# Optimization experiments

Hardware: AMD Instinct MI355X
Metric: run time of the kernel (lower is better)

## Reference

```python
import jax, jax.numpy as jnp
import numpy as np

B, Q, K, A, H, C, O = 32, 512, 512, 256, 8, 32, 256  # batch, queries, keys, channels, heads, head_dim, out_dim


def setup_inputs() -> dict:
    key = jax.random.key(0)
    ks = jax.random.split(key, 12)
    s = 0.02
    return {
        "q_data": jax.random.normal(ks[0], (B, Q, A), jnp.float32),
        "m_data": jax.random.normal(ks[1], (B, K, A), jnp.float32),
        "bias": jax.random.normal(ks[2], (B, 1, 1, K), jnp.float32),
        "nonbatched_bias": jax.random.normal(ks[3], (H, Q, K), jnp.float32),
        "batched_bias": jax.random.normal(ks[4], (B, H, Q, K), jnp.float32),
        "query_w": jax.random.normal(ks[5], (A, H, C), jnp.float32) * s,
        "key_w": jax.random.normal(ks[6], (A, H, C), jnp.float32) * s,
        "value_w": jax.random.normal(ks[7], (A, H, C), jnp.float32) * s,
        "gating_w": jax.random.normal(ks[8], (A, H, C), jnp.float32) * s,
        "gating_b": jnp.ones((H, C), jnp.float32),
        "output_w": jax.random.normal(ks[9], (H, C, O), jnp.float32) * s,
        "output_b": jnp.zeros((O,), jnp.float32),
    }


def reference(q_data, m_data, bias, nonbatched_bias, batched_bias,
              query_w, key_w, value_w, gating_w, gating_b, output_w, output_b):
    key_scale = query_w.shape[-1] ** -0.5
    q = jnp.einsum('bqa,ahc->bqhc', q_data, query_w) * key_scale
    k = jnp.einsum('bka,ahc->bkhc', m_data, key_w)
    v = jnp.einsum('bka,ahc->bkhc', m_data, value_w)
    logits = jnp.einsum('bqhc,bkhc->bhqk', q, k) + bias
    logits = logits + nonbatched_bias[None] + batched_bias
    weights = jax.nn.softmax(logits, axis=-1)
    weighted_avg = jnp.einsum('bhqk,bkhc->bqhc', weights, v)
    gate = jax.nn.sigmoid(jnp.einsum('bqc,chv->bqhv', q_data, gating_w) + gating_b)
    weighted_avg = weighted_avg * gate
    return jnp.einsum('bqhc,hco->bqo', weighted_avg, output_w) + output_b
```

## Files before the change

kernel.cpp:

```cpp
#include <hip/hip_runtime.h>
#include <cstdint>
#include <cstddef>


typedef __attribute__((ext_vector_type(8))) short short8;
typedef __attribute__((ext_vector_type(4))) float f32x4;
typedef __attribute__((ext_vector_type(4))) unsigned int u32x4;
typedef __attribute__((ext_vector_type(2))) unsigned int u32x2;

#define DEVFN static __device__ __forceinline__
#define L2E 1.4426950408889634f

DEVFN float b2f(unsigned int bits16) {
  return __builtin_bit_cast(float, bits16 << 16);
}
DEVFN unsigned int pack2(float a, float b) {
  unsigned int r;
  asm("v_cvt_pk_bf16_f32 %0, %1, %2" : "=v"(r) : "v"(a), "v"(b));
  return r;
}
DEVFN f32x4 mfma16(short8 a, short8 b, f32x4 c) {
  return __builtin_amdgcn_mfma_f32_16x16x32_bf16(a, b, c, 0, 0, 0);
}
#define GLOAD_LDS16_NT(gp, lp)                                     \
  __builtin_amdgcn_global_load_lds(                                \
      (const __attribute__((address_space(1))) void*)(gp),         \
      (__attribute__((address_space(3))) void*)(lp), 16, 0, 2)

__global__ __launch_bounds__(256) void wtrans_kernel(
    const float* __restrict__ qw, const float* __restrict__ kw,
    const float* __restrict__ vw, const float* __restrict__ gw,
    const float* __restrict__ ow,
    unsigned short* __restrict__ wtq, unsigned short* __restrict__ wtk,
    unsigned short* __restrict__ wtv, unsigned short* __restrict__ wtg,
    unsigned short* __restrict__ wt3)
{
  const int matid = blockIdx.x >> 4;
  const int tile  = blockIdx.x & 15;
  const float* src = (matid == 0) ? qw : (matid == 1) ? kw : (matid == 2) ? vw
                   : (matid == 3) ? gw : ow;
  unsigned short* dst = (matid == 0) ? wtq : (matid == 1) ? wtk : (matid == 2) ? wtv
                      : (matid == 3) ? wtg : wt3;
  const int tr = (tile >> 2) * 64, tc = (tile & 3) * 64;
  __shared__ unsigned short T[64 * 72];
  const int t = threadIdx.x;
  {
    const int row = t >> 2, cb = (t & 3) * 16;
#pragma unroll
    for (int ii = 0; ii < 4; ++ii) {
      f32x4 v = *(const f32x4*)&src[(size_t)(tr + row) * 256 + tc + cb + ii * 4];
      u32x2 p; p.x = pack2(v.x, v.y); p.y = pack2(v.z, v.w);
      *(u32x2*)&T[row * 72 + cb + ii * 4] = p;
    }
  }
  __syncthreads();
  {
    const int c0 = t >> 2, rb = (t & 3) * 16;
    unsigned short vals[16];
#pragma unroll
    for (int m = 0; m < 16; ++m) vals[m] = T[(rb + m) * 72 + c0];
    u32x4 s0, s1;
    s0.x = (unsigned)vals[0]  | ((unsigned)vals[1]  << 16);
    s0.y = (unsigned)vals[2]  | ((unsigned)vals[3]  << 16);
    s0.z = (unsigned)vals[4]  | ((unsigned)vals[5]  << 16);
    s0.w = (unsigned)vals[6]  | ((unsigned)vals[7]  << 16);
    s1.x = (unsigned)vals[8]  | ((unsigned)vals[9]  << 16);
    s1.y = (unsigned)vals[10] | ((unsigned)vals[11] << 16);
    s1.z = (unsigned)vals[12] | ((unsigned)vals[13] << 16);
    s1.w = (unsigned)vals[14] | ((unsigned)vals[15] << 16);
    unsigned short* dp = &dst[(size_t)(tc + c0) * 256 + tr + rb];
    *(u32x4*)dp = s0;
    *(u32x4*)(dp + 8) = s1;
  }
}

__global__ __launch_bounds__(512, 4) void proj_kernel(
    const float* __restrict__ q_data, const float* __restrict__ m_data,
    const unsigned short* __restrict__ wtq, const unsigned short* __restrict__ wtk,
    const unsigned short* __restrict__ wtv, const unsigned short* __restrict__ wtg,
    const float* __restrict__ gating_b,
    unsigned short* __restrict__ qp, unsigned short* __restrict__ kp,
    unsigned short* __restrict__ vp, unsigned short* __restrict__ gate)
{
  const int bid = blockIdx.x;
  const bool mside = bid >= 256;
  const int r0 = (mside ? bid - 256 : bid) * 64;
  const float* inp = mside ? m_data : q_data;
  __shared__ unsigned short Alds[64 * 264];
  __shared__ unsigned short Wlds[2][256 * 40];
  const int t = threadIdx.x;
  const int lane = t & 63, wave = t >> 6;
  const int l15 = lane & 15, g = lane >> 4;
  const int stripe = wave & 3, nhalf = wave >> 2;

  {
    const int row = t >> 3, cb = (t & 7) * 32;
    const float* ip = &inp[(size_t)(r0 + row) * 256 + cb];
#pragma unroll
    for (int i = 0; i < 4; ++i) {
      f32x4 a0 = *(const f32x4*)&ip[i * 8];
      f32x4 a1 = *(const f32x4*)&ip[i * 8 + 4];
      u32x4 pk;
      pk.x = pack2(a0.x, a0.y); pk.y = pack2(a0.z, a0.w);
      pk.z = pack2(a1.x, a1.y); pk.w = pack2(a1.z, a1.w);
      *(u32x4*)&Alds[row * 264 + cb + i * 8] = pk;
    }
  }

  const unsigned short* wt0 = mside ? wtk : wtq;
  const unsigned short* wt1 = mside ? wtv : wtg;
  const int wrow = t & 255, whalf = t >> 8;

  {
    const u32x4* wsrc = (const u32x4*)&wt0[(size_t)wrow * 256 + whalf * 16];
    u32x4 a = wsrc[0], b = wsrc[1];
    *(u32x4*)&Wlds[0][wrow * 40 + whalf * 16 + 0] = a;
    *(u32x4*)&Wlds[0][wrow * 40 + whalf * 16 + 8] = b;
  }

  f32x4 acc[8];
#pragma unroll
  for (int j = 0; j < 8; ++j) acc[j] = f32x4{0.f, 0.f, 0.f, 0.f};

  const int arow = (stripe * 16 + l15) * 264 + 8 * g;
  const int grow = r0 + stripe * 16 + l15;
  const int ob = grow >> 9, oq = grow & 511;

#pragma unroll
  for (int s = 0; s < 16; ++s) {
    const int p = s & 1;
    __syncthreads();
    u32x4 nw0, nw1;
    if (s < 15) {
      const unsigned short* wt = (s + 1 < 8) ? wt0 : wt1;
      const u32x4* wsrc =
          (const u32x4*)&wt[(size_t)wrow * 256 + ((s + 1) & 7) * 32 + whalf * 16];
      nw0 = wsrc[0]; nw1 = wsrc[1];
    }
    const int ks = s & 7;
    short8 bf = __builtin_bit_cast(short8, *(const u32x4*)&Alds[arow + ks * 32]);
#pragma unroll
    for (int j = 0; j < 8; ++j) {
      short8 wf = __builtin_bit_cast(short8,
          *(const u32x4*)&Wlds[p][((nhalf * 8 + j) * 16 + l15) * 40 + 8 * g]);
      acc[j] = mfma16(wf, bf, acc[j]);
    }
    if (s < 15) {
      *(u32x4*)&Wlds[p ^ 1][wrow * 40 + whalf * 16 + 0] = nw0;
      *(u32x4*)&Wlds[p ^ 1][wrow * 40 + whalf * 16 + 8] = nw1;
    }
    if (s == 7 || s == 15) {
      const int oi = s >> 3;
      const float QS = 0.17677669529663687f * 1.4426950408889634f;
#pragma unroll
      for (int j = 0; j < 8; ++j) {
        const int n0 = (nhalf * 8 + j) * 16 + 4 * g;
        const int h = n0 >> 5, c0 = n0 & 31;
        const size_t idx = ((size_t)(ob * 8 + h) * 512 + oq) * 32 + c0;
        f32x4 v = acc[j];
        if (!mside) {
          if (oi == 0) {
            u32x2 st;
            st.x = pack2(v.x * QS, v.y * QS);
            st.y = pack2(v.z * QS, v.w * QS);
            *(u32x2*)&qp[idx] = st;
          } else {
            f32x4 gb = *(const f32x4*)&gating_b[n0];
            f32x4 gv;
            gv.x = 1.0f / (1.0f + exp2f(-(v.x + gb.x) * L2E));
            gv.y = 1.0f / (1.0f + exp2f(-(v.y + gb.y) * L2E));
            gv.z = 1.0f / (1.0f + exp2f(-(v.z + gb.z) * L2E));
            gv.w = 1.0f / (1.0f + exp2f(-(v.w + gb.w) * L2E));
            u32x2 st;
            st.x = pack2(gv.x, gv.y); st.y = pack2(gv.z, gv.w);
            *(u32x2*)&gate[idx] = st;
          }
        } else {
          u32x2 st;
          st.x = pack2(v.x, v.y); st.y = pack2(v.z, v.w);
          if (oi == 0) *(u32x2*)&kp[idx] = st;
          else         *(u32x2*)&vp[idx] = st;
        }
        acc[j] = f32x4{0.f, 0.f, 0.f, 0.f};
      }
    }
  }
}

__global__ __launch_bounds__(512, 2) void attn_kernel(
    const unsigned short* __restrict__ qp, const unsigned short* __restrict__ kp,
    const unsigned short* __restrict__ vp,
    const float* __restrict__ bias, const float* __restrict__ nbias,
    const float* __restrict__ bbias,
    unsigned short* __restrict__ wa)
{
  const int bid = blockIdx.x;
  const int h = bid & 7;
  const int b = bid >> 3;
  const int bh = bid;
  const int t = threadIdx.x;
  const int lane = t & 63, wave = t >> 6;
  const int l15 = lane & 15, g = lane >> 4;

  __shared__ unsigned short Klds[512 * 32];
  __shared__ unsigned short Vt[32 * 520];
  __shared__ float Bb[2][8192];
  __shared__ float Bk[512];

  const float* bbb_bh = bbias + (size_t)bh * 262144;
  const int qc = lane >> 3, sl = lane & 7;
  const float* wsrc0 = bbb_bh + (size_t)(wave * 32 + qc) * 512 + ((sl ^ qc) << 2);

#pragma unroll
  for (int i = 0; i < 4; ++i)
    GLOAD_LDS16_NT(wsrc0 + i * 4096,      &Bb[0][(wave * 4 + i) * 256]);
#pragma unroll
  for (int i = 0; i < 4; ++i)
    GLOAD_LDS16_NT(wsrc0 + i * 4096 + 32, &Bb[1][(wave * 4 + i) * 256]);

  {
    const int row = t;
    const u32x4* ks = (const u32x4*)&kp[((size_t)bh * 512 + row) * 32];
    u32x4 k0 = ks[0], k1 = ks[1], k2 = ks[2], k3 = ks[3];
    *(u32x4*)&Klds[row * 32 + 0]  = k0;
    *(u32x4*)&Klds[row * 32 + 8]  = k1;
    *(u32x4*)&Klds[row * 32 + 16] = k2;
    *(u32x4*)&Klds[row * 32 + 24] = k3;
    const u32x4* vs = (const u32x4*)&vp[((size_t)bh * 512 + row) * 32];
#pragma unroll
    for (int cc = 0; cc < 4; ++cc) {
      u32x4 vv = vs[cc];
      unsigned int dw0 = vv.x, dw1 = vv.y, dw2 = vv.z, dw3 = vv.w;
      const int c = cc * 8;
      Vt[(c + 0) * 520 + row] = (unsigned short)(dw0 & 0xffff);
      Vt[(c + 1) * 520 + row] = (unsigned short)(dw0 >> 16);
      Vt[(c + 2) * 520 + row] = (unsigned short)(dw1 & 0xffff);
      Vt[(c + 3) * 520 + row] = (unsigned short)(dw1 >> 16);
      Vt[(c + 4) * 520 + row] = (unsigned short)(dw2 & 0xffff);
      Vt[(c + 5) * 520 + row] = (unsigned short)(dw2 >> 16);
      Vt[(c + 6) * 520 + row] = (unsigned short)(dw3 & 0xffff);
      Vt[(c + 7) * 520 + row] = (unsigned short)(dw3 >> 16);
    }
    if (t < 128) {
      f32x4 bv = *(const f32x4*)&bias[(size_t)b * 512 + t * 4];
      bv.x *= L2E; bv.y *= L2E; bv.z *= L2E; bv.w *= L2E;
      *(f32x4*)&Bk[t * 4] = bv;
    }
  }

  const int pib = ((g & 1) << 4) | ((g >> 1) << 3);
  const bool godd = (g & 1) != 0;
  const int sw0 = (g ^ (l15 & 7)) << 2;
  const int sw1 = ((g + 4) ^ (l15 & 7)) << 2;
  const int bq0 = (wave * 32 + l15) * 32;
  const int bq1 = bq0 + 16 * 32;

  f32x4 Cn00, Cn01, Cn10, Cn11;
  {
    const float* nn = nbias + (size_t)h * 262144
                    + (size_t)(wave * 32 + l15) * 512 + 4 * g;
    Cn00 = *(const f32x4*)nn;
    Cn01 = *(const f32x4*)(nn + 16);
    Cn10 = *(const f32x4*)(nn + 16 * 512);
    Cn11 = *(const f32x4*)(nn + 16 * 512 + 16);
  }

  short8 qf0, qf1;
  f32x4 acc[2][2];
  float l_part[2] = {0.f, 0.f};

  __syncthreads();

  for (int tok = 0; tok < 32; ++tok) {
    const int pass = tok >> 4, kt = tok & 15, p = tok & 1;
    const int k0 = kt * 32;

    if (kt == 0) {
      const int qbase = pass * 256 + wave * 32;
      qf0 = __builtin_bit_cast(short8,
          *(const u32x4*)&qp[((size_t)bh * 512 + qbase + l15) * 32 + 8 * g]);
      qf1 = __builtin_bit_cast(short8,
          *(const u32x4*)&qp[((size_t)bh * 512 + qbase + 16 + l15) * 32 + 8 * g]);
#pragma unroll
      for (int ct = 0; ct < 2; ++ct)
#pragma unroll
        for (int qt = 0; qt < 2; ++qt) acc[ct][qt] = f32x4{0.f, 0.f, 0.f, 0.f};
      l_part[0] = 0.f; l_part[1] = 0.f;
    }

    short8 kf0 = __builtin_bit_cast(short8, *(const u32x4*)&Klds[(k0 + l15) * 32 + 8 * g]);
    short8 kf1 = __builtin_bit_cast(short8, *(const u32x4*)&Klds[(k0 + 16 + l15) * 32 + 8 * g]);
    short8 vf0 = __builtin_bit_cast(short8, *(const u32x4*)&Vt[l15 * 520 + k0 + pib]);
    short8 vf1 = __builtin_bit_cast(short8, *(const u32x4*)&Vt[(16 + l15) * 520 + k0 + pib]);
    f32x4 bks0 = *(const f32x4*)&Bk[k0 + 4 * g];
    f32x4 bks1 = *(const f32x4*)&Bk[k0 + 16 + 4 * g];
    const float* bp = Bb[p];
    f32x4 bb00 = *(const f32x4*)&bp[bq0 + sw0];
    f32x4 bb01 = *(const f32x4*)&bp[bq0 + sw1];
    f32x4 bb10 = *(const f32x4*)&bp[bq1 + sw0];
    f32x4 bb11 = *(const f32x4*)&bp[bq1 + sw1];
    asm volatile("s_waitcnt lgkmcnt(0)" ::: "memory");
    __builtin_amdgcn_sched_barrier(0);

    f32x4 Nn00, Nn01, Nn10, Nn11;
    if (tok < 31) {
      const int nt = tok + 1;
      const float* nn = nbias + (size_t)h * 262144
          + (size_t)((nt >> 4) * 256 + wave * 32 + l15) * 512 + (nt & 15) * 32 + 4 * g;
      Nn00 = *(const f32x4*)nn;
      Nn01 = *(const f32x4*)(nn + 16);
      Nn10 = *(const f32x4*)(nn + 16 * 512);
      Nn11 = *(const f32x4*)(nn + 16 * 512 + 16);
    }

    if (tok < 30) {
      const int ft = tok + 2;
      const float* ws = wsrc0 + (size_t)(ft >> 4) * 131072 + (ft & 15) * 32;
#pragma unroll
      for (int i = 0; i < 4; ++i)
        GLOAD_LDS16_NT(ws + (size_t)i * 4096, &Bb[p][(wave * 4 + i) * 256]);
    }

    __builtin_amdgcn_s_setprio(1);
#pragma unroll
    for (int qt = 0; qt < 2; ++qt) {
      f32x4 bb0 = qt ? bb10 : bb00;
      f32x4 bb1 = qt ? bb11 : bb01;
      f32x4 nb0 = qt ? Cn10 : Cn00;
      f32x4 nb1 = qt ? Cn11 : Cn01;
      f32x4 c0 = bb0 * L2E + (nb0 * L2E + bks0);
      f32x4 c1 = bb1 * L2E + (nb1 * L2E + bks1);
      short8 qf = qt ? qf1 : qf0;
      f32x4 s0 = mfma16(kf0, qf, c0);
      f32x4 s1 = mfma16(kf1, qf, c1);
      f32x4 p0, p1;
      p0.x = exp2f(s0.x); p0.y = exp2f(s0.y);
      p0.z = exp2f(s0.z); p0.w = exp2f(s0.w);
      p1.x = exp2f(s1.x); p1.y = exp2f(s1.y);
      p1.z = exp2f(s1.z); p1.w = exp2f(s1.w);
      l_part[qt] += ((p0.x + p0.y) + (p0.z + p0.w)) +
                    ((p1.x + p1.y) + (p1.z + p1.w));
      unsigned int d0 = pack2(p0.x, p0.y), d1 = pack2(p0.z, p0.w);
      unsigned int e0 = pack2(p1.x, p1.y), e1 = pack2(p1.z, p1.w);
      unsigned int pd0 = __shfl_xor(d0, 16, 64), pd1 = __shfl_xor(d1, 16, 64);
      unsigned int pe0 = __shfl_xor(e0, 16, 64), pe1 = __shfl_xor(e1, 16, 64);
      u32x4 pfu;
      pfu.x = godd ? pe0 : d0;
      pfu.y = godd ? pe1 : d1;
      pfu.z = godd ? e0 : pd0;
      pfu.w = godd ? e1 : pd1;
      short8 pf = __builtin_bit_cast(short8, pfu);
      acc[0][qt] = mfma16(vf0, pf, acc[0][qt]);
      acc[1][qt] = mfma16(vf1, pf, acc[1][qt]);
    }
    __builtin_amdgcn_s_setprio(0);

    if (tok < 31) { Cn00 = Nn00; Cn01 = Nn01; Cn10 = Nn10; Cn11 = Nn11; }

    if (tok < 30)       asm volatile("s_waitcnt vmcnt(8)" ::: "memory");
    else if (tok == 30) asm volatile("s_waitcnt vmcnt(4)" ::: "memory");

    if (kt == 15) {
      const int qbase = pass * 256 + wave * 32;
      unsigned short* wab = wa + (size_t)bh * 512 * 32;
#pragma unroll
      for (int qt = 0; qt < 2; ++qt) {
        float l = l_part[qt];
        l += __shfl_xor(l, 16, 64);
        l += __shfl_xor(l, 32, 64);
        const float rl = 1.0f / l;
        const int q = qbase + qt * 16 + l15;
#pragma unroll
        for (int ct = 0; ct < 2; ++ct) {
          f32x4 v = acc[ct][qt];
          u32x2 st;
          st.x = pack2(v.x * rl, v.y * rl);
          st.y = pack2(v.z * rl, v.w * rl);
          *(u32x2*)&wab[q * 32 + ct * 16 + 4 * g] = st;
        }
      }
    }
  }
}

__global__ __launch_bounds__(256, 2) void outp_kernel(
    const unsigned short* __restrict__ wa, const unsigned short* __restrict__ gate,
    const unsigned short* __restrict__ wt3, const float* __restrict__ out_b,
    float* __restrict__ out)
{
  const int r0 = blockIdx.x * 32;
  const int t = threadIdx.x;
  const int lane = t & 63, wave = t >> 6;
  const int l15 = lane & 15, g = lane >> 4;
  const int stripe = wave & 1, half = wave >> 1;
  __shared__ unsigned short Wlds[2][256 * 40];

  const int grow = r0 + stripe * 16 + l15;
  const int b = grow >> 9, q = grow & 511;

  {
    const u32x4* wsrc = (const u32x4*)&wt3[(size_t)t * 256];
    u32x4 a = wsrc[0], bb = wsrc[1], c = wsrc[2], d = wsrc[3];
    *(u32x4*)&Wlds[0][t * 40 + 0]  = a;
    *(u32x4*)&Wlds[0][t * 40 + 8]  = bb;
    *(u32x4*)&Wlds[0][t * 40 + 16] = c;
    *(u32x4*)&Wlds[0][t * 40 + 24] = d;
  }
  size_t aidx = ((size_t)(b * 8 + 0) * 512 + q) * 32 + 8 * g;
  u32x4 cwv = *(const u32x4*)&wa[aidx];
  u32x4 cgv = *(const u32x4*)&gate[aidx];

  f32x4 acc[8];
#pragma unroll
  for (int j = 0; j < 8; ++j) acc[j] = f32x4{0.f, 0.f, 0.f, 0.f};

#pragma unroll
  for (int s = 0; s < 8; ++s) {
    const int p = s & 1;
    __syncthreads();
    u32x4 nw0, nw1, nw2, nw3, nwv, ngv;
    if (s < 7) {
      const u32x4* wsrc = (const u32x4*)&wt3[(size_t)t * 256 + (s + 1) * 32];
      nw0 = wsrc[0]; nw1 = wsrc[1]; nw2 = wsrc[2]; nw3 = wsrc[3];
      const size_t na = ((size_t)(b * 8 + s + 1) * 512 + q) * 32 + 8 * g;
      nwv = *(const u32x4*)&wa[na];
      ngv = *(const u32x4*)&gate[na];
    }
    float f0 = b2f(cwv.x & 0xffff) * b2f(cgv.x & 0xffff);
    float f1 = b2f(cwv.x >> 16)    * b2f(cgv.x >> 16);
    float f2 = b2f(cwv.y & 0xffff) * b2f(cgv.y & 0xffff);
    float f3 = b2f(cwv.y >> 16)    * b2f(cgv.y >> 16);
    float f4 = b2f(cwv.z & 0xffff) * b2f(cgv.z & 0xffff);
    float f5 = b2f(cwv.z >> 16)    * b2f(cgv.z >> 16);
    float f6 = b2f(cwv.w & 0xffff) * b2f(cgv.w & 0xffff);
    float f7 = b2f(cwv.w >> 16)    * b2f(cgv.w >> 16);
    u32x4 au;
    au.x = pack2(f0, f1); au.y = pack2(f2, f3);
    au.z = pack2(f4, f5); au.w = pack2(f6, f7);
    short8 af = __builtin_bit_cast(short8, au);
#pragma unroll
    for (int j = 0; j < 8; ++j) {
      short8 wf = __builtin_bit_cast(short8,
          *(const u32x4*)&Wlds[p][((half * 8 + j) * 16 + l15) * 40 + 8 * g]);
      acc[j] = mfma16(wf, af, acc[j]);
    }
    if (s < 7) {
      *(u32x4*)&Wlds[p ^ 1][t * 40 + 0]  = nw0;
      *(u32x4*)&Wlds[p ^ 1][t * 40 + 8]  = nw1;
      *(u32x4*)&Wlds[p ^ 1][t * 40 + 16] = nw2;
      *(u32x4*)&Wlds[p ^ 1][t * 40 + 24] = nw3;
      cwv = nwv; cgv = ngv;
    }
  }
#pragma unroll
  for (int j = 0; j < 8; ++j) {
    const int o0 = (half * 8 + j) * 16 + 4 * g;
    f32x4 ob4 = *(const f32x4*)&out_b[o0];
    f32x4 v = acc[j] + ob4;
    *(f32x4*)&out[(size_t)grow * 256 + o0] = v;
  }
}

extern "C" void kernel_launch(void* const* d_in, const int* in_sizes, int n_in,
                              void* d_out, int out_size, void* d_ws, size_t ws_size,
                              hipStream_t stream)
{
  const float* q_data   = (const float*)d_in[0];
  const float* m_data   = (const float*)d_in[1];
  const float* bias     = (const float*)d_in[2];
  const float* nbb      = (const float*)d_in[3];
  const float* bbb      = (const float*)d_in[4];
  const float* query_w  = (const float*)d_in[5];
  const float* key_w    = (const float*)d_in[6];
  const float* value_w  = (const float*)d_in[7];
  const float* gating_w = (const float*)d_in[8];
  const float* gating_b = (const float*)d_in[9];
  const float* output_w = (const float*)d_in[10];
  const float* output_b = (const float*)d_in[11];
  float* out = (float*)d_out;

  const size_t QP_B   = (size_t)32 * 8 * 512 * 32 * 2;
  const size_t GATE_B = (size_t)32 * 8 * 512 * 32 * 2;
  const size_t WT_B   = (size_t)256 * 256 * 2;

  char* ws = (char*)d_ws;
  unsigned short* qp  = (unsigned short*)(ws);
  unsigned short* kp  = (unsigned short*)(ws + QP_B);
  unsigned short* vp  = (unsigned short*)(ws + 2 * QP_B);
  unsigned short* wab = (unsigned short*)(ws + 3 * QP_B);
  unsigned short* gat = (unsigned short*)(ws + 4 * QP_B);
  unsigned short* wtq = (unsigned short*)(ws + 4 * QP_B + GATE_B);
  unsigned short* wtk = (unsigned short*)(ws + 4 * QP_B + GATE_B + WT_B);
  unsigned short* wtv = (unsigned short*)(ws + 4 * QP_B + GATE_B + 2 * WT_B);
  unsigned short* wtg = (unsigned short*)(ws + 4 * QP_B + GATE_B + 3 * WT_B);
  unsigned short* wt3 = (unsigned short*)(ws + 4 * QP_B + GATE_B + 4 * WT_B);
  const size_t need = 4 * QP_B + GATE_B + 5 * WT_B;
  if (ws_size < need) return;

  hipLaunchKernelGGL(wtrans_kernel, dim3(80), dim3(256), 0, stream,
                     query_w, key_w, value_w, gating_w, output_w,
                     wtq, wtk, wtv, wtg, wt3);
  hipLaunchKernelGGL(proj_kernel, dim3(512), dim3(512), 0, stream,
                     q_data, m_data, wtq, wtk, wtv, wtg, gating_b,
                     qp, kp, vp, gat);
  hipLaunchKernelGGL(attn_kernel, dim3(256), dim3(512), 0, stream,
                     qp, kp, vp, bias, nbb, bbb, wab);
  hipLaunchKernelGGL(outp_kernel, dim3(512), dim3(256), 0, stream,
                     wab, gat, wt3, output_b, out);
}
```

Baseline: 120.5 us.

## Widen key tile to 64 and single-buffer batched-bias staging in LDS

The attention main loop now handles 64 keys per iteration instead of 32, halving the trip count to 16. Each iteration issues four QK MFMAs and two PV MFMA pairs per query tile. The batched-bias staging changes from a double-buffered 32-column LDS layout to one 64-column per-wave buffer with a new XOR swizzle. The next tile is prefetched into that buffer after the current values are read into registers. The aim is to amortise per-iteration waits, loop overhead and load issue across more work. The cost is higher register use under 512-thread, 2-block launch bounds, a risk of spills, and a prefetch distance cut from two tiles to one.

New measurement: 121.1 us. About the same (+0.5%).

```diff
diff --git a/kernel.cpp b/kernel.cpp
--- a/kernel.cpp
+++ b/kernel.cpp
@@ -204,19 +204,17 @@
 
   __shared__ unsigned short Klds[512 * 32];
   __shared__ unsigned short Vt[32 * 520];
-  __shared__ float Bb[2][8192];
+  __shared__ float Bt[256 * 64];
   __shared__ float Bk[512];
 
   const float* bbb_bh = bbias + (size_t)bh * 262144;
-  const int qc = lane >> 3, sl = lane & 7;
-  const float* wsrc0 = bbb_bh + (size_t)(wave * 32 + qc) * 512 + ((sl ^ qc) << 2);
-
-#pragma unroll
-  for (int i = 0; i < 4; ++i)
-    GLOAD_LDS16_NT(wsrc0 + i * 4096,      &Bb[0][(wave * 4 + i) * 256]);
-#pragma unroll
-  for (int i = 0; i < 4; ++i)
-    GLOAD_LDS16_NT(wsrc0 + i * 4096 + 32, &Bb[1][(wave * 4 + i) * 256]);
+  const int qc4 = lane >> 4, sl16 = lane & 15;
+  const float* wbase = bbb_bh + (size_t)(wave * 32 + qc4) * 512;
+
+#pragma unroll
+  for (int c = 0; c < 8; ++c)
+    GLOAD_LDS16_NT(wbase + (size_t)(c * 4) * 512 + ((sl16 ^ ((c * 4 + qc4) & 15)) << 2),
+                   &Bt[(wave * 32 + c * 4) * 64]);
 
   {
     const int row = t;
@@ -250,32 +248,32 @@
 
   const int pib = ((g & 1) << 4) | ((g >> 1) << 3);
   const bool godd = (g & 1) != 0;
-  const int sw0 = (g ^ (l15 & 7)) << 2;
-  const int sw1 = ((g + 4) ^ (l15 & 7)) << 2;
-  const int bq0 = (wave * 32 + l15) * 32;
-  const int bq1 = bq0 + 16 * 32;
-
-  f32x4 Cn00, Cn01, Cn10, Cn11;
-  {
-    const float* nn = nbias + (size_t)h * 262144
-                    + (size_t)(wave * 32 + l15) * 512 + 4 * g;
-    Cn00 = *(const f32x4*)nn;
-    Cn01 = *(const f32x4*)(nn + 16);
-    Cn10 = *(const f32x4*)(nn + 16 * 512);
-    Cn11 = *(const f32x4*)(nn + 16 * 512 + 16);
+  const int tr0 = (wave * 32 + l15) * 64;
+  const int tr1 = tr0 + 16 * 64;
+
+  f32x4 Cn[2][4];
+  {
+    const float* nn0 = nbias + (size_t)h * 262144
+                     + (size_t)(wave * 32 + l15) * 512 + 4 * g;
+#pragma unroll
+    for (int qt = 0; qt < 2; ++qt)
+#pragma unroll
+      for (int kk = 0; kk < 4; ++kk)
+        Cn[qt][kk] = *(const f32x4*)(nn0 + (size_t)qt * 16 * 512 + kk * 16);
   }
 
   short8 qf0, qf1;
   f32x4 acc[2][2];
   float l_part[2] = {0.f, 0.f};
 
+  asm volatile("s_waitcnt vmcnt(0)" ::: "memory");
   __syncthreads();
 
-  for (int tok = 0; tok < 32; ++tok) {
-    const int pass = tok >> 4, kt = tok & 15, p = tok & 1;
-    const int k0 = kt * 32;
-
-    if (kt == 0) {
+  for (int tok = 0; tok < 16; ++tok) {
+    const int pass = tok >> 3, kt8 = tok & 7;
+    const int k0 = kt8 * 64;
+
+    if (kt8 == 0) {
       const int qbase = pass * 256 + wave * 32;
       qf0 = __builtin_bit_cast(short8,
           *(const u32x4*)&qp[((size_t)bh * 512 + qbase + l15) * 32 + 8 * g]);
@@ -288,79 +286,91 @@
       l_part[0] = 0.f; l_part[1] = 0.f;
     }
 
-    short8 kf0 = __builtin_bit_cast(short8, *(const u32x4*)&Klds[(k0 + l15) * 32 + 8 * g]);
-    short8 kf1 = __builtin_bit_cast(short8, *(const u32x4*)&Klds[(k0 + 16 + l15) * 32 + 8 * g]);
-    short8 vf0 = __builtin_bit_cast(short8, *(const u32x4*)&Vt[l15 * 520 + k0 + pib]);
-    short8 vf1 = __builtin_bit_cast(short8, *(const u32x4*)&Vt[(16 + l15) * 520 + k0 + pib]);
-    f32x4 bks0 = *(const f32x4*)&Bk[k0 + 4 * g];
-    f32x4 bks1 = *(const f32x4*)&Bk[k0 + 16 + 4 * g];
-    const float* bp = Bb[p];
-    f32x4 bb00 = *(const f32x4*)&bp[bq0 + sw0];
-    f32x4 bb01 = *(const f32x4*)&bp[bq0 + sw1];
-    f32x4 bb10 = *(const f32x4*)&bp[bq1 + sw0];
-    f32x4 bb11 = *(const f32x4*)&bp[bq1 + sw1];
+    short8 kf[4], vf[2][2];
+    f32x4 bks[4], bb0[4], bb1[4];
+#pragma unroll
+    for (int kk = 0; kk < 4; ++kk) {
+      kf[kk] = __builtin_bit_cast(short8,
+          *(const u32x4*)&Klds[(k0 + kk * 16 + l15) * 32 + 8 * g]);
+      bks[kk] = *(const f32x4*)&Bk[k0 + kk * 16 + 4 * g];
+      const int slot = ((kk * 4 + g) ^ l15) << 2;
+      bb0[kk] = *(const f32x4*)&Bt[tr0 + slot];
+      bb1[kk] = *(const f32x4*)&Bt[tr1 + slot];
+    }
+#pragma unroll
+    for (int ks = 0; ks < 2; ++ks) {
+      vf[0][ks] = __builtin_bit_cast(short8,
+          *(const u32x4*)&Vt[l15 * 520 + k0 + ks * 32 + pib]);
+      vf[1][ks] = __builtin_bit_cast(short8,
+          *(const u32x4*)&Vt[(16 + l15) * 520 + k0 + ks * 32 + pib]);
+    }
     asm volatile("s_waitcnt lgkmcnt(0)" ::: "memory");
     __builtin_amdgcn_sched_barrier(0);
 
-    f32x4 Nn00, Nn01, Nn10, Nn11;
-    if (tok < 31) {
+    if (tok < 15) {
+      const int ft = tok + 1;
+      const float* ws = wbase + (size_t)(ft >> 3) * 131072 + (ft & 7) * 64;
+#pragma unroll
+      for (int c = 0; c < 8; ++c)
+        GLOAD_LDS16_NT(ws + (size_t)(c * 4) * 512 + ((sl16 ^ ((c * 4 + qc4) & 15)) << 2),
+                       &Bt[(wave * 32 + c * 4) * 64]);
+    }
+    f32x4 Nn[2][4];
+    if (tok < 15) {
       const int nt = tok + 1;
-      const float* nn = nbias + (size_t)h * 262144
-          + (size_t)((nt >> 4) * 256 + wave * 32 + l15) * 512 + (nt & 15) * 32 + 4 * g;
-      Nn00 = *(const f32x4*)nn;
-      Nn01 = *(const f32x4*)(nn + 16);
-      Nn10 = *(const f32x4*)(nn + 16 * 512);
-      Nn11 = *(const f32x4*)(nn + 16 * 512 + 16);
-    }
-
-    if (tok < 30) {
-      const int ft = tok + 2;
-      const float* ws = wsrc0 + (size_t)(ft >> 4) * 131072 + (ft & 15) * 32;
-#pragma unroll
-      for (int i = 0; i < 4; ++i)
-        GLOAD_LDS16_NT(ws + (size_t)i * 4096, &Bb[p][(wave * 4 + i) * 256]);
+      const float* nn0 = nbias + (size_t)h * 262144
+          + (size_t)((nt >> 3) * 256 + wave * 32 + l15) * 512 + (nt & 7) * 64 + 4 * g;
+#pragma unroll
+      for (int qt = 0; qt < 2; ++qt)
+#pragma unroll
+        for (int kk = 0; kk < 4; ++kk)
+          Nn[qt][kk] = *(const f32x4*)(nn0 + (size_t)qt * 16 * 512 + kk * 16);
     }
 
     __builtin_amdgcn_s_setprio(1);
 #pragma unroll
     for (int qt = 0; qt < 2; ++qt) {
-      f32x4 bb0 = qt ? bb10 : bb00;
-      f32x4 bb1 = qt ? bb11 : bb01;
-      f32x4 nb0 = qt ? Cn10 : Cn00;
-      f32x4 nb1 = qt ? Cn11 : Cn01;
-      f32x4 c0 = bb0 * L2E + (nb0 * L2E + bks0);
-      f32x4 c1 = bb1 * L2E + (nb1 * L2E + bks1);
       short8 qf = qt ? qf1 : qf0;
-      f32x4 s0 = mfma16(kf0, qf, c0);
-      f32x4 s1 = mfma16(kf1, qf, c1);
-      f32x4 p0, p1;
-      p0.x = exp2f(s0.x); p0.y = exp2f(s0.y);
-      p0.z = exp2f(s0.z); p0.w = exp2f(s0.w);
-      p1.x = exp2f(s1.x); p1.y = exp2f(s1.y);
-      p1.z = exp2f(s1.z); p1.w = exp2f(s1.w);
-      l_part[qt] += ((p0.x + p0.y) + (p0.z + p0.w)) +
-                    ((p1.x + p1.y) + (p1.z + p1.w));
-      unsigned int d0 = pack2(p0.x, p0.y), d1 = pack2(p0.z, p0.w);
-      unsigned int e0 = pack2(p1.x, p1.y), e1 = pack2(p1.z, p1.w);
-      unsigned int pd0 = __shfl_xor(d0, 16, 64), pd1 = __shfl_xor(d1, 16, 64);
-      unsigned int pe0 = __shfl_xor(e0, 16, 64), pe1 = __shfl_xor(e1, 16, 64);
-      u32x4 pfu;
-      pfu.x = godd ? pe0 : d0;
-      pfu.y = godd ? pe1 : d1;
-      pfu.z = godd ? e0 : pd0;
-      pfu.w = godd ? e1 : pd1;
-      short8 pf = __builtin_bit_cast(short8, pfu);
-      acc[0][qt] = mfma16(vf0, pf, acc[0][qt]);
-      acc[1][qt] = mfma16(vf1, pf, acc[1][qt]);
+      f32x4 pr[4];
+#pragma unroll
+      for (int kk = 0; kk < 4; ++kk) {
+        f32x4 bb = qt ? bb1[kk] : bb0[kk];
+        f32x4 c = bb * L2E + (Cn[qt][kk] * L2E + bks[kk]);
+        f32x4 s = mfma16(kf[kk], qf, c);
+        f32x4 pe;
+        pe.x = exp2f(s.x); pe.y = exp2f(s.y);
+        pe.z = exp2f(s.z); pe.w = exp2f(s.w);
+        l_part[qt] += (pe.x + pe.y) + (pe.z + pe.w);
+        pr[kk] = pe;
+      }
+#pragma unroll
+      for (int ks = 0; ks < 2; ++ks) {
+        f32x4 p0 = pr[2 * ks], p1 = pr[2 * ks + 1];
+        unsigned int d0 = pack2(p0.x, p0.y), d1 = pack2(p0.z, p0.w);
+        unsigned int e0 = pack2(p1.x, p1.y), e1 = pack2(p1.z, p1.w);
+        unsigned int pd0 = __shfl_xor(d0, 16, 64), pd1 = __shfl_xor(d1, 16, 64);
+        unsigned int pe0 = __shfl_xor(e0, 16, 64), pe1 = __shfl_xor(e1, 16, 64);
+        u32x4 pfu;
+        pfu.x = godd ? pe0 : d0;
+        pfu.y = godd ? pe1 : d1;
+        pfu.z = godd ? e0 : pd0;
+        pfu.w = godd ? e1 : pd1;
+        short8 pf = __builtin_bit_cast(short8, pfu);
+        acc[0][qt] = mfma16(vf[0][ks], pf, acc[0][qt]);
+        acc[1][qt] = mfma16(vf[1][ks], pf, acc[1][qt]);
+      }
     }
     __builtin_amdgcn_s_setprio(0);
 
-    if (tok < 31) { Cn00 = Nn00; Cn01 = Nn01; Cn10 = Nn10; Cn11 = Nn11; }
-
-    if (tok < 30)       asm volatile("s_waitcnt vmcnt(8)" ::: "memory");
-    else if (tok == 30) asm volatile("s_waitcnt vmcnt(4)" ::: "memory");
-
-    if (kt == 15) {
+#pragma unroll
+    for (int qt = 0; qt < 2; ++qt)
+#pragma unroll
+      for (int kk = 0; kk < 4; ++kk)
+        if (tok < 15) Cn[qt][kk] = Nn[qt][kk];
+
+    if (tok < 15) asm volatile("s_waitcnt vmcnt(8)" ::: "memory");
+
+    if (kt8 == 7) {
       const int qbase = pass * 256 + wave * 32;
       unsigned short* wab = wa + (size_t)bh * 512 * 32;
 #pragma unroll
```
